# Optimization experiments

Measured on AMD Instinct MI355X. Metric: run time of the kernel, lower is better.

## Reference

```python
import jax, jax.numpy as jnp
import numpy as np

B, TT, TA, H = 2, 128, 512, 1024
EPS = 1e-5


def _conv1d(x, w, b, pad):
    # x: [B, C_in, T], w: [C_out, C_in, K] -> [B, C_out, T]
    y = jax.lax.conv_general_dilated(x, w, window_strides=(1,), padding=[(pad, pad)],
                                     dimension_numbers=('NCH', 'OIH', 'NCH'))
    return y + b[None, :, None]


def _groupnorm1(x, g, b):
    # GroupNorm(num_groups=1): normalize over (C, T) per sample. x: [B, C, T]
    mu = jnp.mean(x, axis=(1, 2), keepdims=True)
    var = jnp.var(x, axis=(1, 2), keepdims=True)
    xn = (x - mu) * jax.lax.rsqrt(var + EPS)
    return xn * g[None, :, None] + b[None, :, None]


def setup_inputs() -> dict:
    key = jax.random.key(0)
    ks = jax.random.split(key, 16)
    s = 0.02
    return {
        'text_hidden': jax.random.normal(ks[0], (B, TT, H), jnp.float32),
        'audio_hidden': jax.random.normal(ks[1], (B, TA, H), jnp.float32),
        # alignment_proj: Linear(2H, H) -> ReLU -> Linear(H, 1)
        'a_w1': jax.random.normal(ks[2], (2 * H, H), jnp.float32) * s,
        'a_b1': jnp.zeros((H,), jnp.float32),
        'a_w2': jax.random.normal(ks[3], (H, 1), jnp.float32) * s,
        'a_b2': jnp.zeros((1,), jnp.float32),
        # duration_predictor: Conv1d(H,H,3) ReLU GN(1,H) Conv1d(H,H,3) ReLU GN(1,H) Conv1d(H,1,1)
        'd_w1': jax.random.normal(ks[4], (H, H, 3), jnp.float32) * s,
        'd_b1': jnp.zeros((H,), jnp.float32),
        'gn1_g': jnp.ones((H,), jnp.float32),
        'gn1_b': jnp.zeros((H,), jnp.float32),
        'd_w2': jax.random.normal(ks[5], (H, H, 3), jnp.float32) * s,
        'd_b2': jnp.zeros((H,), jnp.float32),
        'gn2_g': jnp.ones((H,), jnp.float32),
        'gn2_b': jnp.zeros((H,), jnp.float32),
        'd_w3': jax.random.normal(ks[6], (1, H, 1), jnp.float32) * s,
        'd_b3': jnp.zeros((1,), jnp.float32),
    }


def reference(text_hidden, audio_hidden, a_w1, a_b1, a_w2, a_b2,
              d_w1, d_b1, gn1_g, gn1_b, d_w2, d_b2, gn2_g, gn2_b, d_w3, d_b3):
    # ---- predict_durations ----
    x = jnp.swapaxes(text_hidden, 1, 2)                      # [B, H, TT]
    x = _groupnorm1(jax.nn.relu(_conv1d(x, d_w1, d_b1, 1)), gn1_g, gn1_b)
    x = _groupnorm1(jax.nn.relu(_conv1d(x, d_w2, d_b2, 1)), gn2_g, gn2_b)
    x = _conv1d(x, d_w3, d_b3, 0)                            # [B, 1, TT]
    durations = jax.nn.softplus(x[:, 0, :])                  # [B, TT]

    # ---- soft_mas (temperature = 1.0) ----
    # Linear on concat([text, audio]) == text @ W1[:H] + audio @ W1[H:] + b1
    t_part = jnp.einsum('bth,hd->btd', text_hidden, a_w1[:H])    # [B, TT, H]
    a_part = jnp.einsum('bah,hd->bad', audio_hidden, a_w1[H:])   # [B, TA, H]
    hid = jax.nn.relu(t_part[:, :, None, :] + a_part[:, None, :, :] + a_b1)  # [B,TT,TA,H]
    logits = jnp.einsum('btad,do->bta', hid, a_w2) + a_b2[0]     # [B, TT, TA]

    pos = jnp.arange(TA, dtype=logits.dtype)                     # audio positions j
    expected = jnp.arange(TT, dtype=logits.dtype) * (TA / TT)    # expected pos per text i
    monotonic_bias = -0.1 * jnp.abs(pos[None, :] - expected[:, None])  # [TT, TA]
    logits = logits + monotonic_bias[None, :, :]

    alignment = jax.nn.softmax(logits, axis=-1)
    return alignment, durations
```

## Files before the change

### kernel.cpp

```cpp
#include <hip/hip_runtime.h>
#include <hip/hip_bf16.h>


typedef __bf16 bf16_t;
typedef __bf16 bf16x8 __attribute__((ext_vector_type(8)));
typedef __bf16 bf16x4 __attribute__((ext_vector_type(4)));
typedef float  f32x4  __attribute__((ext_vector_type(4)));
typedef _Float16 f16_t;
typedef _Float16 f16x2 __attribute__((ext_vector_type(2)));
typedef _Float16 f16x4 __attribute__((ext_vector_type(4)));

#define EPSV 1e-5f

#define OFF_TEXTBF   0u
#define OFF_AUDIOBF  524288u
#define OFF_W1TOP    2621440u
#define OFF_W1BOT    4718592u
#define OFF_WC1      6815744u
#define OFF_WC2      13107200u
#define OFF_TP       19398656u
#define OFF_W2F      19922944u
#define OFF_APT      20447232u
#define OFF_XP0      22544384u
#define OFF_XP1      23076864u
#define OFF_Y2       23609344u
#define OFF_BST1     24133632u
#define OFF_BST2     24137728u
#define OFF_LP       24141824u
#define OFF_SG       26238976u
#define OFF_SB       26251264u

__global__ __launch_bounds__(256) void prep_k(
    const float* __restrict__ text, const float* __restrict__ audio,
    const float* __restrict__ w1,
    const float* __restrict__ w1c, const float* __restrict__ w2c,
    const float* __restrict__ w2,
    const float* __restrict__ g1, const float* __restrict__ b1g,
    bf16_t* __restrict__ text_bf, bf16_t* __restrict__ xp0,
    bf16_t* __restrict__ audio_bf,
    bf16_t* __restrict__ topT, bf16_t* __restrict__ botT,
    bf16_t* __restrict__ wc1, bf16_t* __restrict__ wc2,
    bf16_t* __restrict__ xp1, f16_t* __restrict__ w2f,
    float* __restrict__ Sg, float* __restrict__ Sb)
{
    __shared__ float tile[32][33];
    const int bid = blockIdx.x;
    if (bid < 1280) {
        const int e = (bid * 256 + threadIdx.x) * 4;
        if (e < 262144) {
            float4 v = *(const float4*)&text[e];
            bf16x4 o; o[0] = (bf16_t)v.x; o[1] = (bf16_t)v.y; o[2] = (bf16_t)v.z; o[3] = (bf16_t)v.w;
            *(bf16x4*)&text_bf[e] = o;
            const int bt = e >> 10, h = e & 1023;
            const int b = bt >> 7, t = bt & 127;
            *(bf16x4*)&xp0[(size_t)(b * 130 + 1 + t) * 1024 + h] = o;
        } else {
            const int ea = e - 262144;
            float4 v = *(const float4*)&audio[ea];
            bf16x4 o; o[0] = (bf16_t)v.x; o[1] = (bf16_t)v.y; o[2] = (bf16_t)v.z; o[3] = (bf16_t)v.w;
            *(bf16x4*)&audio_bf[ea] = o;
        }
    } else if (bid < 3328) {
        const int b2 = bid - 1280;
        const int bx = b2 & 31, by = b2 >> 5;
        const int tx = threadIdx.x & 31, ty = threadIdx.x >> 5;
        #pragma unroll
        for (int j = 0; j < 4; ++j)
            tile[ty + j * 8][tx] = w1[(size_t)(by * 32 + ty + j * 8) * 1024 + bx * 32 + tx];
        __syncthreads();
        bf16_t* out = (by < 32) ? topT : botT;
        const int hbase = (by & 31) * 32;
        #pragma unroll
        for (int j = 0; j < 4; ++j) {
            const int d = bx * 32 + ty + j * 8;
            out[(size_t)d * 1024 + hbase + tx] = (bf16_t)tile[tx][ty + j * 8];
        }
    } else if (bid < 5376) {
        int b2 = bid - 3328;
        const int is2 = (b2 >= 1024) ? 1 : 0;
        const float* w = is2 ? w2c : w1c;
        bf16_t* wc = is2 ? wc2 : wc1;
        b2 &= 1023;
        const int o = b2, i4 = threadIdx.x;
        const float* src = w + (size_t)o * 3072 + i4 * 12;
        float4 v0 = *(const float4*)&src[0];
        float4 v1 = *(const float4*)&src[4];
        float4 v2 = *(const float4*)&src[8];
        const float f[12] = {v0.x, v0.y, v0.z, v0.w, v1.x, v1.y, v1.z, v1.w, v2.x, v2.y, v2.z, v2.w};
        float g4[4] = {1.f, 1.f, 1.f, 1.f}, bb4[4] = {0.f, 0.f, 0.f, 0.f};
        if (is2) {
            float4 gv = *(const float4*)&g1[i4 * 4];
            float4 bv = *(const float4*)&b1g[i4 * 4];
            g4[0] = gv.x; g4[1] = gv.y; g4[2] = gv.z; g4[3] = gv.w;
            bb4[0] = bv.x; bb4[1] = bv.y; bb4[2] = bv.z; bb4[3] = bv.w;
        }
        float sgr[3] = {0.f, 0.f, 0.f}, sbr[3] = {0.f, 0.f, 0.f};
        #pragma unroll
        for (int r = 0; r < 3; ++r) {
            bf16x4 o4;
            #pragma unroll
            for (int j = 0; j < 4; ++j) {
                const float wv = f[j * 3 + r];
                const float ws = wv * g4[j];
                sgr[r] += ws;
                sbr[r] += wv * bb4[j];
                o4[j] = (bf16_t)(is2 ? ws : wv);
            }
            *(bf16x4*)&wc[(size_t)r * 1048576 + (size_t)o * 1024 + i4 * 4] = o4;
        }
        if (is2) {
            #pragma unroll
            for (int off = 32; off > 0; off >>= 1) {
                #pragma unroll
                for (int r = 0; r < 3; ++r) {
                    sgr[r] += __shfl_xor(sgr[r], off);
                    sbr[r] += __shfl_xor(sbr[r], off);
                }
            }
            float* red = &tile[0][0];
            const int wid = threadIdx.x >> 6, lane = threadIdx.x & 63;
            if (lane == 0) {
                #pragma unroll
                for (int r = 0; r < 3; ++r) {
                    red[wid * 6 + r] = sgr[r];
                    red[wid * 6 + 3 + r] = sbr[r];
                }
            }
            __syncthreads();
            if (threadIdx.x < 6) {
                const float v = red[threadIdx.x] + red[6 + threadIdx.x]
                              + red[12 + threadIdx.x] + red[18 + threadIdx.x];
                if (threadIdx.x < 3) Sg[o * 3 + threadIdx.x] = v;
                else                 Sb[o * 3 + threadIdx.x - 3] = v;
            }
        }
    } else {
        const int tid = threadIdx.x;
        const int rowmap[4] = {0, 129, 130, 259};
        const int f = tid * 16;
        const int r = f >> 10, w = f & 1023;
        bf16x8 z8 = (bf16x8)(bf16_t)0.0f;
        bf16_t* p0 = xp0 + (size_t)rowmap[r] * 1024 + w;
        bf16_t* p1 = xp1 + (size_t)rowmap[r] * 1024 + w;
        *(bf16x8*)p0 = z8; *(bf16x8*)(p0 + 8) = z8;
        *(bf16x8*)p1 = z8; *(bf16x8*)(p1 + 8) = z8;
        float4 wv = *(const float4*)&w2[tid * 4];
        f16x4 wo; wo[0] = (f16_t)wv.x; wo[1] = (f16_t)wv.y; wo[2] = (f16_t)wv.z; wo[3] = (f16_t)wv.w;
        *(f16x4*)&w2f[tid * 4] = wo;
    }
}

__device__ __forceinline__ void conv_tile(
    const bf16_t* __restrict__ Wc, const bf16_t* __restrict__ xp,
    const float* __restrict__ bias, bf16_t* __restrict__ out,
    int rowsPerB, int rowOff, float* __restrict__ bstat, int statIdx,
    int bx, int by, int tid, float* smem, float* sred, float* sredq)
{
    const int w = tid >> 6, l = tid & 63;
    const int bt0 = bx * 32, m0 = by * 16;
    const int i0 = w * 128;
    const int lm = l & 15, lk = (l >> 4) * 8;
    const int b = bt0 >> 7, tbase = bt0 & 127;
    f32x4 acc0 = (f32x4)(0.0f), acc1 = (f32x4)(0.0f);
    const bf16_t* aq = Wc + (size_t)(m0 + lm) * 1024 + i0 + lk;
    const bf16_t* bq = xp + (size_t)(b * 130 + tbase + lm) * 1024 + i0 + lk;
    #pragma unroll
    for (int r = 0; r < 3; ++r) {
        const bf16_t* ar = aq + (size_t)r * 1048576;
        const bf16_t* br = bq + (size_t)r * 1024;
        #pragma unroll
        for (int kk = 0; kk < 128; kk += 32) {
            bf16x8 af = *(const bf16x8*)(ar + kk);
            bf16x8 bf0 = *(const bf16x8*)(br + kk);
            bf16x8 bf1 = *(const bf16x8*)(br + 16384 + kk);
            acc0 = __builtin_amdgcn_mfma_f32_16x16x32_bf16(af, bf0, acc0, 0, 0, 0);
            acc1 = __builtin_amdgcn_mfma_f32_16x16x32_bf16(af, bf1, acc1, 0, 0, 0);
        }
    }
    {
        const int row = (l >> 4) * 4;
        #pragma unroll
        for (int r = 0; r < 4; ++r) {
            smem[w * 576 + (row + r) * 36 + lm] = acc0[r];
            smem[w * 576 + (row + r) * 36 + 16 + lm] = acc1[r];
        }
    }
    __syncthreads();
    const int m = tid >> 5, n = tid & 31;
    float v = 0.f;
    #pragma unroll
    for (int ww = 0; ww < 8; ++ww) v += smem[ww * 576 + m * 36 + n];
    v = fmaxf(v + bias[m0 + m], 0.f);
    float s = v, q = v * v;
    __syncthreads();
    smem[m * 36 + n] = v;
    #pragma unroll
    for (int off = 32; off > 0; off >>= 1) {
        s += __shfl_xor(s, off);
        q += __shfl_xor(q, off);
    }
    if (l == 0) { sred[w] = s; sredq[w] = q; }
    __syncthreads();
    if (tid == 0) {
        float ts = 0.f, tq = 0.f;
        #pragma unroll
        for (int ww = 0; ww < 8; ++ww) { ts += sred[ww]; tq += sredq[ww]; }
        bstat[statIdx * 2] = ts;
        bstat[statIdx * 2 + 1] = tq;
    }
    if (tid < 64) {
        const int row = tid >> 1, half = tid & 1;
        bf16x8 o8;
        #pragma unroll
        for (int j = 0; j < 8; ++j) o8[j] = (bf16_t)smem[(half * 8 + j) * 36 + row];
        const int t = tbase + row;
        *(bf16x8*)&out[(size_t)(b * rowsPerB + rowOff + t) * 1024 + m0 + half * 8] = o8;
    }
}

__device__ __forceinline__ void reduce_bstat(
    const float* __restrict__ bstat, int b, int tid,
    float* sr, float* sq, float& mu, float& rsig)
{
    const int lane = tid & 63, wid = tid >> 6;
    float s = 0.f, q = 0.f;
    if (tid < 256) {
        float2 v = ((const float2*)bstat)[b * 256 + tid];
        s = v.x; q = v.y;
    }
    #pragma unroll
    for (int off = 32; off > 0; off >>= 1) {
        s += __shfl_xor(s, off);
        q += __shfl_xor(q, off);
    }
    if (lane == 0) { sr[wid] = s; sq[wid] = q; }
    __syncthreads();
    float ts = 0.f, tq = 0.f;
    #pragma unroll
    for (int i = 0; i < 8; ++i) { ts += sr[i]; tq += sq[i]; }
    const float cnt = 131072.f;
    mu = ts / cnt;
    const float var = tq / cnt - mu * mu;
    rsig = rsqrtf(var + EPSV);
}

__device__ __forceinline__ void conv2_tile(
    const bf16_t* __restrict__ Wc, const bf16_t* __restrict__ xp,
    const float* __restrict__ bias, bf16_t* __restrict__ out,
    const float* __restrict__ bstat1,
    const float* __restrict__ Sg, const float* __restrict__ Sb,
    float* __restrict__ bstat2, int statIdx,
    int bx, int by, int tid, float* smem, float* sred, float* sredq,
    float* sr, float* sq)
{
    const int w = tid >> 6, l = tid & 63;
    const int bt0 = bx * 32, m0 = by * 16;
    const int i0 = w * 128;
    const int lm = l & 15, lk = (l >> 4) * 8;
    const int b = bt0 >> 7, tbase = bt0 & 127;
    float mu1, rsig1;
    reduce_bstat(bstat1, b, tid, sr, sq, mu1, rsig1);
    f32x4 acc0 = (f32x4)(0.0f), acc1 = (f32x4)(0.0f);
    const bf16_t* aq = Wc + (size_t)(m0 + lm) * 1024 + i0 + lk;
    const bf16_t* bq = xp + (size_t)(b * 130 + tbase + lm) * 1024 + i0 + lk;
    #pragma unroll
    for (int r = 0; r < 3; ++r) {
        const bf16_t* ar = aq + (size_t)r * 1048576;
        const bf16_t* br = bq + (size_t)r * 1024;
        #pragma unroll
        for (int kk = 0; kk < 128; kk += 32) {
            bf16x8 af = *(const bf16x8*)(ar + kk);
            bf16x8 bf0 = *(const bf16x8*)(br + kk);
            bf16x8 bf1 = *(const bf16x8*)(br + 16384 + kk);
            acc0 = __builtin_amdgcn_mfma_f32_16x16x32_bf16(af, bf0, acc0, 0, 0, 0);
            acc1 = __builtin_amdgcn_mfma_f32_16x16x32_bf16(af, bf1, acc1, 0, 0, 0);
        }
    }
    {
        const int row = (l >> 4) * 4;
        #pragma unroll
        for (int r = 0; r < 4; ++r) {
            smem[w * 576 + (row + r) * 36 + lm] = acc0[r];
            smem[w * 576 + (row + r) * 36 + 16 + lm] = acc1[r];
        }
    }
    __syncthreads();
    const int m = tid >> 5, n = tid & 31;
    float v = 0.f;
    #pragma unroll
    for (int ww = 0; ww < 8; ++ww) v += smem[ww * 576 + m * 36 + n];
    const int o = m0 + m;
    const int tloc = tbase + n;
    float sb = Sb[o * 3] + Sb[o * 3 + 1] + Sb[o * 3 + 2];
    float sg = Sg[o * 3] + Sg[o * 3 + 1] + Sg[o * 3 + 2];
    if (tloc == 0)   { sb -= Sb[o * 3];     sg -= Sg[o * 3]; }
    if (tloc == 127) { sb -= Sb[o * 3 + 2]; sg -= Sg[o * 3 + 2]; }
    v = fmaxf(rsig1 * v + sb - mu1 * rsig1 * sg + bias[o], 0.f);
    float s = v, q = v * v;
    __syncthreads();
    smem[m * 36 + n] = v;
    #pragma unroll
    for (int off = 32; off > 0; off >>= 1) {
        s += __shfl_xor(s, off);
        q += __shfl_xor(q, off);
    }
    if (l == 0) { sred[w] = s; sredq[w] = q; }
    __syncthreads();
    if (tid == 0) {
        float ts = 0.f, tq = 0.f;
        #pragma unroll
        for (int ww = 0; ww < 8; ++ww) { ts += sred[ww]; tq += sredq[ww]; }
        bstat2[statIdx * 2] = ts;
        bstat2[statIdx * 2 + 1] = tq;
    }
    if (tid < 64) {
        const int row = tid >> 1, half = tid & 1;
        bf16x8 o8;
        #pragma unroll
        for (int j = 0; j < 8; ++j) o8[j] = (bf16_t)smem[(half * 8 + j) * 36 + row];
        const int t = tbase + row;
        *(bf16x8*)&out[(size_t)(b * 128 + t) * 1024 + m0 + half * 8] = o8;
    }
}

__device__ __forceinline__ void gemm_unit(
    int unit, int ut, float* base,
    const bf16_t* __restrict__ text_bf, const bf16_t* __restrict__ w1topT,
    const float* __restrict__ b1, f16_t* __restrict__ tp,
    const bf16_t* __restrict__ audio_bf, const bf16_t* __restrict__ w1botT,
    f16_t* __restrict__ apT4)
{
    const int is_tp = (unit < 256) ? 1 : 0;
    const int b2 = is_tp ? unit : unit - 256;
    const int n0 = (b2 & 31) * 32, m0 = (b2 >> 5) * 32;
    const int w = ut >> 6, l = ut & 63;
    const int lm = l & 15, lk = (l >> 4) * 8;
    const int k0 = w * 256;
    const bf16_t* A  = is_tp ? text_bf : audio_bf;
    const bf16_t* Bt = is_tp ? w1topT : w1botT;
    f32x4 acc[2][2];
    #pragma unroll
    for (int mt = 0; mt < 2; ++mt)
        #pragma unroll
        for (int nt = 0; nt < 2; ++nt) acc[mt][nt] = (f32x4)(0.0f);
    const bf16_t* Ap = A + (size_t)(m0 + lm) * 1024 + k0 + lk;
    const bf16_t* Bp = Bt + (size_t)(n0 + lm) * 1024 + k0 + lk;
    #pragma unroll
    for (int kk = 0; kk < 256; kk += 32) {
        bf16x8 af[2], bfr[2];
        #pragma unroll
        for (int i = 0; i < 2; ++i) af[i] = *(const bf16x8*)(Ap + (size_t)i * 16384 + kk);
        #pragma unroll
        for (int i = 0; i < 2; ++i) bfr[i] = *(const bf16x8*)(Bp + (size_t)i * 16384 + kk);
        #pragma unroll
        for (int mt = 0; mt < 2; ++mt)
            #pragma unroll
            for (int nt = 0; nt < 2; ++nt)
                acc[mt][nt] = __builtin_amdgcn_mfma_f32_16x16x32_bf16(af[mt], bfr[nt], acc[mt][nt], 0, 0, 0);
    }
    #pragma unroll
    for (int mt = 0; mt < 2; ++mt) {
        const int row = mt * 16 + (l >> 4) * 4;
        #pragma unroll
        for (int nt = 0; nt < 2; ++nt)
            #pragma unroll
            for (int r = 0; r < 4; ++r)
                base[w * 1152 + (row + r) * 36 + nt * 16 + lm] = acc[mt][nt][r];
    }
    __syncthreads();
    if (is_tp) {
        const int m = ut >> 3, n4 = (ut & 7) * 4;
        f16x4 v;
        #pragma unroll
        for (int j = 0; j < 4; ++j)
            v[j] = (f16_t)(base[m * 36 + n4 + j] + base[1152 + m * 36 + n4 + j]
                         + base[2304 + m * 36 + n4 + j] + base[3456 + m * 36 + n4 + j]
                         + b1[n0 + n4 + j]);
        *(f16x4*)&tp[(size_t)(m0 + m) * 1024 + n0 + n4] = v;
    } else {
        const int a = ut >> 3, q = ut & 7;
        const int b = m0 >> 9, a0 = m0 & 511;
        f16x4 v;
        #pragma unroll
        for (int c = 0; c < 4; ++c)
            v[c] = (f16_t)(base[a * 36 + q * 4 + c] + base[1152 + a * 36 + q * 4 + c]
                         + base[2304 + a * 36 + q * 4 + c] + base[3456 + a * 36 + q * 4 + c]);
        const size_t hq = (size_t)(n0 >> 2) + q;
        *(f16x4*)&apT4[(hq * 1024 + b * 512 + a0 + a) * 4] = v;
    }
}

__global__ __launch_bounds__(512, 4) void p2_k(
    const bf16_t* __restrict__ wc1, const bf16_t* __restrict__ xp0,
    const float* __restrict__ d_b1, bf16_t* __restrict__ xp1,
    float* __restrict__ bstat1,
    const bf16_t* __restrict__ text_bf, const bf16_t* __restrict__ w1topT,
    const float* __restrict__ a_b1, f16_t* __restrict__ tp,
    const bf16_t* __restrict__ audio_bf, const bf16_t* __restrict__ w1botT,
    f16_t* __restrict__ apT4)
{
    __shared__ float smem[9216];
    __shared__ float sred[8], sredq[8];
    const int bid = blockIdx.x;
    const int tid = threadIdx.x;
    if (bid < 512) {
        conv_tile(wc1, xp0, d_b1, xp1, 130, 1, bstat1, bid,
                  bid >> 6, bid & 63, tid, smem, sred, sredq);
    } else {
        const int unit = (bid - 512) * 2 + (tid >> 8);
        gemm_unit(unit, tid & 255, smem + (tid >> 8) * 4608,
                  text_bf, w1topT, a_b1, tp, audio_bf, w1botT, apT4);
    }
}

__device__ __forceinline__ float dot2_acc(f16x2 x, f16x2 w, float acc) {
#if __has_builtin(__builtin_amdgcn_fdot2)
    return __builtin_amdgcn_fdot2(x, w, acc, false);
#else
    return acc + (float)x[0] * (float)w[0] + (float)x[1] * (float)w[1];
#endif
}

__global__ __launch_bounds__(512, 4) void p3_k(
    const bf16_t* __restrict__ wc2, const bf16_t* __restrict__ xp1,
    const float* __restrict__ d_b2, bf16_t* __restrict__ y2,
    float* __restrict__ bstat2, const float* __restrict__ bstat1,
    const float* __restrict__ Sg, const float* __restrict__ Sb,
    const f16_t* __restrict__ tp, const f16_t* __restrict__ apT4,
    const f16_t* __restrict__ w2f, float* __restrict__ lp)
{
    __shared__ float smem[4608];
    __shared__ float sred[8], sredq[8], sr[8], sq[8];
    const int bid = blockIdx.x;
    const int tid = threadIdx.x;
    if (bid < 512) {
        conv2_tile(wc2, xp1, d_b2, y2, bstat1, Sg, Sb, bstat2, bid,
                   bid >> 6, bid & 63, tid, smem, sred, sredq, sr, sq);
    } else {
        const int lb = bid - 512;
        const int btp = lb & 63, hc = lb >> 6;
        const int bt0 = btp * 4;
        const int b = bt0 >> 7;
        const int a = tid;
        const f16_t* tpr = tp + (size_t)bt0 * 1024 + hc * 256;
        const f16_t* w2r = w2f + hc * 256;
        const f16_t* apc = apT4 + ((size_t)(hc * 64) * 1024 + b * 512 + a) * 4;
        float acc[4] = {0.f, 0.f, 0.f, 0.f};
        const f16x2 zero = (f16x2)(f16_t)0.0f;
        #pragma unroll 2
        for (int hq = 0; hq < 64; hq += 2) {
            f16x4 a0 = *(const f16x4*)(apc + (size_t)hq * 4096);
            f16x4 a1 = *(const f16x4*)(apc + (size_t)(hq + 1) * 4096);
            f16x4 w0 = *(const f16x4*)&w2r[hq * 4];
            f16x4 w1 = *(const f16x4*)&w2r[hq * 4 + 4];
            #pragma unroll
            for (int r = 0; r < 4; ++r) {
                f16x4 t0 = *(const f16x4*)&tpr[r * 1024 + hq * 4];
                f16x4 t1 = *(const f16x4*)&tpr[r * 1024 + hq * 4 + 4];
                f16x2 p;
                p = __builtin_elementwise_max((f16x2){t0[0] + a0[0], t0[1] + a0[1]}, zero);
                acc[r] = dot2_acc(p, (f16x2){w0[0], w0[1]}, acc[r]);
                p = __builtin_elementwise_max((f16x2){t0[2] + a0[2], t0[3] + a0[3]}, zero);
                acc[r] = dot2_acc(p, (f16x2){w0[2], w0[3]}, acc[r]);
                p = __builtin_elementwise_max((f16x2){t1[0] + a1[0], t1[1] + a1[1]}, zero);
                acc[r] = dot2_acc(p, (f16x2){w1[0], w1[1]}, acc[r]);
                p = __builtin_elementwise_max((f16x2){t1[2] + a1[2], t1[3] + a1[3]}, zero);
                acc[r] = dot2_acc(p, (f16x2){w1[2], w1[3]}, acc[r]);
            }
        }
        float* dst = lp + (size_t)(hc * 256 + bt0) * 512 + a;
        #pragma unroll
        for (int r = 0; r < 4; ++r) dst[(size_t)r * 512] = acc[r];
    }
}

__global__ __launch_bounds__(512) void combine_k(
    const float* __restrict__ lp, const float* __restrict__ b2,
    const bf16_t* __restrict__ y2, const float* __restrict__ bstat2,
    const float* __restrict__ g, const float* __restrict__ bet,
    const float* __restrict__ w3, const float* __restrict__ b3,
    float* __restrict__ out)
{
    __shared__ float redm[8], redsum[8];
    const int bid = blockIdx.x;
    const int tid = threadIdx.x;
    if (bid < 256) {
        const int bt = bid, t = bt & 127;
        const int a = tid;
        const int lane = a & 63, wid = a >> 6;
        const size_t base = (size_t)bt * 512 + a;
        float v = lp[base] + lp[131072 + base] + lp[262144 + base] + lp[393216 + base];
        v += b2[0] - 0.1f * fabsf((float)a - 4.0f * (float)t);
        float m = v;
        #pragma unroll
        for (int off = 32; off > 0; off >>= 1) m = fmaxf(m, __shfl_xor(m, off));
        if (lane == 0) redm[wid] = m;
        __syncthreads();
        float M = redm[0];
        #pragma unroll
        for (int i = 1; i < 8; ++i) M = fmaxf(M, redm[i]);
        const float e = expf(v - M);
        float s = e;
        #pragma unroll
        for (int off = 32; off > 0; off >>= 1) s += __shfl_xor(s, off);
        if (lane == 0) redsum[wid] = s;
        __syncthreads();
        float S = redsum[0];
        #pragma unroll
        for (int i = 1; i < 8; ++i) S += redsum[i];
        out[(size_t)bt * 512 + a] = e * (1.0f / S);
    } else {
        const int cb = bid - 256;
        const int b = (cb * 8) >> 7;
        float mu, rsig;
        reduce_bstat(bstat2, b, tid, redm, redsum, mu, rsig);
        const int lane = tid & 63, w = tid >> 6;
        const int bt = cb * 8 + w;
        const bf16_t* row = y2 + (size_t)bt * 1024 + lane * 16;
        float s1 = 0.f, s2 = 0.f, s3 = 0.f;
        #pragma unroll
        for (int c = 0; c < 2; ++c) {
            bf16x8 yv = *(const bf16x8*)(row + c * 8);
            #pragma unroll
            for (int j = 0; j < 8; ++j) {
                const int i = lane * 16 + c * 8 + j;
                const float gw = g[i] * w3[i];
                s1 += gw * (float)yv[j];
                s2 += gw;
                s3 += bet[i] * w3[i];
            }
        }
        #pragma unroll
        for (int off = 32; off > 0; off >>= 1) {
            s1 += __shfl_xor(s1, off);
            s2 += __shfl_xor(s2, off);
            s3 += __shfl_xor(s3, off);
        }
        if (lane == 0) {
            const float t = rsig * (s1 - mu * s2) + s3 + b3[0];
            out[131072 + bt] = fmaxf(t, 0.f) + log1pf(expf(-fabsf(t)));
        }
    }
}

extern "C" void kernel_launch(void* const* d_in, const int* in_sizes, int n_in,
                              void* d_out, int out_size, void* d_ws, size_t ws_size,
                              hipStream_t stream) {
    const float* text   = (const float*)d_in[0];
    const float* audio  = (const float*)d_in[1];
    const float* a_w1   = (const float*)d_in[2];
    const float* a_b1   = (const float*)d_in[3];
    const float* a_w2   = (const float*)d_in[4];
    const float* a_b2   = (const float*)d_in[5];
    const float* d_w1   = (const float*)d_in[6];
    const float* d_b1   = (const float*)d_in[7];
    const float* gn1_g  = (const float*)d_in[8];
    const float* gn1_b  = (const float*)d_in[9];
    const float* d_w2   = (const float*)d_in[10];
    const float* d_b2   = (const float*)d_in[11];
    const float* gn2_g  = (const float*)d_in[12];
    const float* gn2_b  = (const float*)d_in[13];
    const float* d_w3   = (const float*)d_in[14];
    const float* d_b3   = (const float*)d_in[15];

    char* ws = (char*)d_ws;
    float* outf = (float*)d_out;

    bf16_t* text_bf  = (bf16_t*)(ws + OFF_TEXTBF);
    bf16_t* audio_bf = (bf16_t*)(ws + OFF_AUDIOBF);
    bf16_t* w1topT   = (bf16_t*)(ws + OFF_W1TOP);
    bf16_t* w1botT   = (bf16_t*)(ws + OFF_W1BOT);
    bf16_t* wc1      = (bf16_t*)(ws + OFF_WC1);
    bf16_t* wc2      = (bf16_t*)(ws + OFF_WC2);
    f16_t*  tp       = (f16_t*) (ws + OFF_TP);
    f16_t*  w2f      = (f16_t*) (ws + OFF_W2F);
    f16_t*  apT4     = (f16_t*) (ws + OFF_APT);
    bf16_t* xp0      = (bf16_t*)(ws + OFF_XP0);
    bf16_t* xp1      = (bf16_t*)(ws + OFF_XP1);
    bf16_t* y2       = (bf16_t*)(ws + OFF_Y2);
    float*  bstat1   = (float*) (ws + OFF_BST1);
    float*  bstat2   = (float*) (ws + OFF_BST2);
    float*  lp       = (float*) (ws + OFF_LP);
    float*  Sgp      = (float*) (ws + OFF_SG);
    float*  Sbp      = (float*) (ws + OFF_SB);

    prep_k<<<dim3(5377), 256, 0, stream>>>(text, audio, a_w1, d_w1, d_w2, a_w2,
                                           gn1_g, gn1_b,
                                           text_bf, xp0, audio_bf, w1topT, w1botT,
                                           wc1, wc2, xp1, w2f, Sgp, Sbp);
    p2_k<<<dim3(1152), 512, 0, stream>>>(wc1, xp0, d_b1, xp1, bstat1,
                                         text_bf, w1topT, a_b1, tp,
                                         audio_bf, w1botT, apT4);
    p3_k<<<dim3(768), 512, 0, stream>>>(wc2, xp1, d_b2, y2, bstat2, bstat1,
                                        Sgp, Sbp, tp, apT4, w2f, lp);
    combine_k<<<dim3(288), 512, 0, stream>>>(lp, a_b2, y2, bstat2,
                                             gn2_g, gn2_b, d_w3, d_b3, outf);
}
```

Baseline: 181.6 us.

## Replace split-K block GEMMs with one full-K tile per wave, no LDS reduction

Measured after the change: 207.4 us. 1.14x slower.

```diff
diff --git a/kernel.cpp b/kernel.cpp
--- a/kernel.cpp
+++ b/kernel.cpp
@@ -29,6 +29,8 @@
 #define OFF_LP       24141824u
 #define OFF_SG       26238976u
 #define OFF_SB       26251264u
+#define OFF_SGF      26263552u
+#define OFF_SBF      26267648u
 
 __global__ __launch_bounds__(256) void prep_k(
     const float* __restrict__ text, const float* __restrict__ audio,
@@ -41,7 +43,8 @@
     bf16_t* __restrict__ topT, bf16_t* __restrict__ botT,
     bf16_t* __restrict__ wc1, bf16_t* __restrict__ wc2,
     bf16_t* __restrict__ xp1, f16_t* __restrict__ w2f,
-    float* __restrict__ Sg, float* __restrict__ Sb)
+    float* __restrict__ Sg, float* __restrict__ Sb,
+    float* __restrict__ SgF, float* __restrict__ SbF)
 {
     __shared__ float tile[32][33];
     const int bid = blockIdx.x;
@@ -132,7 +135,11 @@
                               + red[12 + threadIdx.x] + red[18 + threadIdx.x];
                 if (threadIdx.x < 3) Sg[o * 3 + threadIdx.x] = v;
                 else                 Sb[o * 3 + threadIdx.x - 3] = v;
-            }
+                red[24 + threadIdx.x] = v;
+            }
+            __syncthreads();
+            if (threadIdx.x == 0)      SgF[o] = red[24] + red[25] + red[26];
+            else if (threadIdx.x == 1) SbF[o] = red[27] + red[28] + red[29];
         }
     } else {
         const int tid = threadIdx.x;
@@ -150,26 +157,25 @@
     }
 }
 
-__device__ __forceinline__ void conv_tile(
+__device__ __forceinline__ float wave_red_add(float v) {
+    #pragma unroll
+    for (int off = 32; off > 0; off >>= 1) v += __shfl_xor(v, off);
+    return v;
+}
+
+__device__ __forceinline__ void conv_mfma(
     const bf16_t* __restrict__ Wc, const bf16_t* __restrict__ xp,
-    const float* __restrict__ bias, bf16_t* __restrict__ out,
-    int rowsPerB, int rowOff, float* __restrict__ bstat, int statIdx,
-    int bx, int by, int tid, float* smem, float* sred, float* sredq)
+    int m0, int b, int tbase, int l, f32x4& acc0, f32x4& acc1)
 {
-    const int w = tid >> 6, l = tid & 63;
-    const int bt0 = bx * 32, m0 = by * 16;
-    const int i0 = w * 128;
     const int lm = l & 15, lk = (l >> 4) * 8;
-    const int b = bt0 >> 7, tbase = bt0 & 127;
-    f32x4 acc0 = (f32x4)(0.0f), acc1 = (f32x4)(0.0f);
-    const bf16_t* aq = Wc + (size_t)(m0 + lm) * 1024 + i0 + lk;
-    const bf16_t* bq = xp + (size_t)(b * 130 + tbase + lm) * 1024 + i0 + lk;
+    const bf16_t* aq = Wc + (size_t)(m0 + lm) * 1024 + lk;
+    const bf16_t* bq = xp + (size_t)(b * 130 + tbase + lm) * 1024 + lk;
     #pragma unroll
     for (int r = 0; r < 3; ++r) {
         const bf16_t* ar = aq + (size_t)r * 1048576;
         const bf16_t* br = bq + (size_t)r * 1024;
-        #pragma unroll
-        for (int kk = 0; kk < 128; kk += 32) {
+        #pragma unroll 4
+        for (int kk = 0; kk < 1024; kk += 32) {
             bf16x8 af = *(const bf16x8*)(ar + kk);
             bf16x8 bf0 = *(const bf16x8*)(br + kk);
             bf16x8 bf1 = *(const bf16x8*)(br + 16384 + kk);
@@ -177,220 +183,9 @@
             acc1 = __builtin_amdgcn_mfma_f32_16x16x32_bf16(af, bf1, acc1, 0, 0, 0);
         }
     }
-    {
-        const int row = (l >> 4) * 4;
-        #pragma unroll
-        for (int r = 0; r < 4; ++r) {
-            smem[w * 576 + (row + r) * 36 + lm] = acc0[r];
-            smem[w * 576 + (row + r) * 36 + 16 + lm] = acc1[r];
-        }
-    }
-    __syncthreads();
-    const int m = tid >> 5, n = tid & 31;
-    float v = 0.f;
-    #pragma unroll
-    for (int ww = 0; ww < 8; ++ww) v += smem[ww * 576 + m * 36 + n];
-    v = fmaxf(v + bias[m0 + m], 0.f);
-    float s = v, q = v * v;
-    __syncthreads();
-    smem[m * 36 + n] = v;
-    #pragma unroll
-    for (int off = 32; off > 0; off >>= 1) {
-        s += __shfl_xor(s, off);
-        q += __shfl_xor(q, off);
-    }
-    if (l == 0) { sred[w] = s; sredq[w] = q; }
-    __syncthreads();
-    if (tid == 0) {
-        float ts = 0.f, tq = 0.f;
-        #pragma unroll
-        for (int ww = 0; ww < 8; ++ww) { ts += sred[ww]; tq += sredq[ww]; }
-        bstat[statIdx * 2] = ts;
-        bstat[statIdx * 2 + 1] = tq;
-    }
-    if (tid < 64) {
-        const int row = tid >> 1, half = tid & 1;
-        bf16x8 o8;
-        #pragma unroll
-        for (int j = 0; j < 8; ++j) o8[j] = (bf16_t)smem[(half * 8 + j) * 36 + row];
-        const int t = tbase + row;
-        *(bf16x8*)&out[(size_t)(b * rowsPerB + rowOff + t) * 1024 + m0 + half * 8] = o8;
-    }
-}
-
-__device__ __forceinline__ void reduce_bstat(
-    const float* __restrict__ bstat, int b, int tid,
-    float* sr, float* sq, float& mu, float& rsig)
-{
-    const int lane = tid & 63, wid = tid >> 6;
-    float s = 0.f, q = 0.f;
-    if (tid < 256) {
-        float2 v = ((const float2*)bstat)[b * 256 + tid];
-        s = v.x; q = v.y;
-    }
-    #pragma unroll
-    for (int off = 32; off > 0; off >>= 1) {
-        s += __shfl_xor(s, off);
-        q += __shfl_xor(q, off);
-    }
-    if (lane == 0) { sr[wid] = s; sq[wid] = q; }
-    __syncthreads();
-    float ts = 0.f, tq = 0.f;
-    #pragma unroll
-    for (int i = 0; i < 8; ++i) { ts += sr[i]; tq += sq[i]; }
-    const float cnt = 131072.f;
-    mu = ts / cnt;
-    const float var = tq / cnt - mu * mu;
-    rsig = rsqrtf(var + EPSV);
-}
-
-__device__ __forceinline__ void conv2_tile(
-    const bf16_t* __restrict__ Wc, const bf16_t* __restrict__ xp,
-    const float* __restrict__ bias, bf16_t* __restrict__ out,
-    const float* __restrict__ bstat1,
-    const float* __restrict__ Sg, const float* __restrict__ Sb,
-    float* __restrict__ bstat2, int statIdx,
-    int bx, int by, int tid, float* smem, float* sred, float* sredq,
-    float* sr, float* sq)
-{
-    const int w = tid >> 6, l = tid & 63;
-    const int bt0 = bx * 32, m0 = by * 16;
-    const int i0 = w * 128;
-    const int lm = l & 15, lk = (l >> 4) * 8;
-    const int b = bt0 >> 7, tbase = bt0 & 127;
-    float mu1, rsig1;
-    reduce_bstat(bstat1, b, tid, sr, sq, mu1, rsig1);
-    f32x4 acc0 = (f32x4)(0.0f), acc1 = (f32x4)(0.0f);
-    const bf16_t* aq = Wc + (size_t)(m0 + lm) * 1024 + i0 + lk;
-    const bf16_t* bq = xp + (size_t)(b * 130 + tbase + lm) * 1024 + i0 + lk;
-    #pragma unroll
-    for (int r = 0; r < 3; ++r) {
-        const bf16_t* ar = aq + (size_t)r * 1048576;
-        const bf16_t* br = bq + (size_t)r * 1024;
-        #pragma unroll
-        for (int kk = 0; kk < 128; kk += 32) {
-            bf16x8 af = *(const bf16x8*)(ar + kk);
-            bf16x8 bf0 = *(const bf16x8*)(br + kk);
-            bf16x8 bf1 = *(const bf16x8*)(br + 16384 + kk);
-            acc0 = __builtin_amdgcn_mfma_f32_16x16x32_bf16(af, bf0, acc0, 0, 0, 0);
-            acc1 = __builtin_amdgcn_mfma_f32_16x16x32_bf16(af, bf1, acc1, 0, 0, 0);
-        }
-    }
-    {
-        const int row = (l >> 4) * 4;
-        #pragma unroll
-        for (int r = 0; r < 4; ++r) {
-            smem[w * 576 + (row + r) * 36 + lm] = acc0[r];
-            smem[w * 576 + (row + r) * 36 + 16 + lm] = acc1[r];
-        }
-    }
-    __syncthreads();
-    const int m = tid >> 5, n = tid & 31;
-    float v = 0.f;
-    #pragma unroll
-    for (int ww = 0; ww < 8; ++ww) v += smem[ww * 576 + m * 36 + n];
-    const int o = m0 + m;
-    const int tloc = tbase + n;
-    float sb = Sb[o * 3] + Sb[o * 3 + 1] + Sb[o * 3 + 2];
-    float sg = Sg[o * 3] + Sg[o * 3 + 1] + Sg[o * 3 + 2];
-    if (tloc == 0)   { sb -= Sb[o * 3];     sg -= Sg[o * 3]; }
-    if (tloc == 127) { sb -= Sb[o * 3 + 2]; sg -= Sg[o * 3 + 2]; }
-    v = fmaxf(rsig1 * v + sb - mu1 * rsig1 * sg + bias[o], 0.f);
-    float s = v, q = v * v;
-    __syncthreads();
-    smem[m * 36 + n] = v;
-    #pragma unroll
-    for (int off = 32; off > 0; off >>= 1) {
-        s += __shfl_xor(s, off);
-        q += __shfl_xor(q, off);
-    }
-    if (l == 0) { sred[w] = s; sredq[w] = q; }
-    __syncthreads();
-    if (tid == 0) {
-        float ts = 0.f, tq = 0.f;
-        #pragma unroll
-        for (int ww = 0; ww < 8; ++ww) { ts += sred[ww]; tq += sredq[ww]; }
-        bstat2[statIdx * 2] = ts;
-        bstat2[statIdx * 2 + 1] = tq;
-    }
-    if (tid < 64) {
-        const int row = tid >> 1, half = tid & 1;
-        bf16x8 o8;
-        #pragma unroll
-        for (int j = 0; j < 8; ++j) o8[j] = (bf16_t)smem[(half * 8 + j) * 36 + row];
-        const int t = tbase + row;
-        *(bf16x8*)&out[(size_t)(b * 128 + t) * 1024 + m0 + half * 8] = o8;
-    }
-}
-
-__device__ __forceinline__ void gemm_unit(
-    int unit, int ut, float* base,
-    const bf16_t* __restrict__ text_bf, const bf16_t* __restrict__ w1topT,
-    const float* __restrict__ b1, f16_t* __restrict__ tp,
-    const bf16_t* __restrict__ audio_bf, const bf16_t* __restrict__ w1botT,
-    f16_t* __restrict__ apT4)
-{
-    const int is_tp = (unit < 256) ? 1 : 0;
-    const int b2 = is_tp ? unit : unit - 256;
-    const int n0 = (b2 & 31) * 32, m0 = (b2 >> 5) * 32;
-    const int w = ut >> 6, l = ut & 63;
-    const int lm = l & 15, lk = (l >> 4) * 8;
-    const int k0 = w * 256;
-    const bf16_t* A  = is_tp ? text_bf : audio_bf;
-    const bf16_t* Bt = is_tp ? w1topT : w1botT;
-    f32x4 acc[2][2];
-    #pragma unroll
-    for (int mt = 0; mt < 2; ++mt)
-        #pragma unroll
-        for (int nt = 0; nt < 2; ++nt) acc[mt][nt] = (f32x4)(0.0f);
-    const bf16_t* Ap = A + (size_t)(m0 + lm) * 1024 + k0 + lk;
-    const bf16_t* Bp = Bt + (size_t)(n0 + lm) * 1024 + k0 + lk;
-    #pragma unroll
-    for (int kk = 0; kk < 256; kk += 32) {
-        bf16x8 af[2], bfr[2];
-        #pragma unroll
-        for (int i = 0; i < 2; ++i) af[i] = *(const bf16x8*)(Ap + (size_t)i * 16384 + kk);
-        #pragma unroll
-        for (int i = 0; i < 2; ++i) bfr[i] = *(const bf16x8*)(Bp + (size_t)i * 16384 + kk);
-        #pragma unroll
-        for (int mt = 0; mt < 2; ++mt)
-            #pragma unroll
-            for (int nt = 0; nt < 2; ++nt)
-                acc[mt][nt] = __builtin_amdgcn_mfma_f32_16x16x32_bf16(af[mt], bfr[nt], acc[mt][nt], 0, 0, 0);
-    }
-    #pragma unroll
-    for (int mt = 0; mt < 2; ++mt) {
-        const int row = mt * 16 + (l >> 4) * 4;
-        #pragma unroll
-        for (int nt = 0; nt < 2; ++nt)
-            #pragma unroll
-            for (int r = 0; r < 4; ++r)
-                base[w * 1152 + (row + r) * 36 + nt * 16 + lm] = acc[mt][nt][r];
-    }
-    __syncthreads();
-    if (is_tp) {
-        const int m = ut >> 3, n4 = (ut & 7) * 4;
-        f16x4 v;
-        #pragma unroll
-        for (int j = 0; j < 4; ++j)
-            v[j] = (f16_t)(base[m * 36 + n4 + j] + base[1152 + m * 36 + n4 + j]
-                         + base[2304 + m * 36 + n4 + j] + base[3456 + m * 36 + n4 + j]
-                         + b1[n0 + n4 + j]);
-        *(f16x4*)&tp[(size_t)(m0 + m) * 1024 + n0 + n4] = v;
-    } else {
-        const int a = ut >> 3, q = ut & 7;
-        const int b = m0 >> 9, a0 = m0 & 511;
-        f16x4 v;
-        #pragma unroll
-        for (int c = 0; c < 4; ++c)
-            v[c] = (f16_t)(base[a * 36 + q * 4 + c] + base[1152 + a * 36 + q * 4 + c]
-                         + base[2304 + a * 36 + q * 4 + c] + base[3456 + a * 36 + q * 4 + c]);
-        const size_t hq = (size_t)(n0 >> 2) + q;
-        *(f16x4*)&apT4[(hq * 1024 + b * 512 + a0 + a) * 4] = v;
-    }
-}
-
-__global__ __launch_bounds__(512, 4) void p2_k(
+}
+
+__global__ __launch_bounds__(256) void p2_k(
     const bf16_t* __restrict__ wc1, const bf16_t* __restrict__ xp0,
     const float* __restrict__ d_b1, bf16_t* __restrict__ xp1,
     float* __restrict__ bstat1,
@@ -399,17 +194,93 @@
     const bf16_t* __restrict__ audio_bf, const bf16_t* __restrict__ w1botT,
     f16_t* __restrict__ apT4)
 {
-    __shared__ float smem[9216];
-    __shared__ float sred[8], sredq[8];
     const int bid = blockIdx.x;
-    const int tid = threadIdx.x;
-    if (bid < 512) {
-        conv_tile(wc1, xp0, d_b1, xp1, 130, 1, bstat1, bid,
-                  bid >> 6, bid & 63, tid, smem, sred, sredq);
+    const int wv = threadIdx.x >> 6, l = threadIdx.x & 63;
+    const int lm = l & 15, lh = l >> 4, lk = lh * 8;
+    if (bid < 128) {
+        const int tile = bid * 4 + wv;
+        const int bx = tile >> 6, by = tile & 63;
+        const int bt0 = bx * 32, m0 = by * 16;
+        const int b = bt0 >> 7, tbase = bt0 & 127;
+        f32x4 acc0 = (f32x4)(0.0f), acc1 = (f32x4)(0.0f);
+        conv_mfma(wc1, xp0, m0, b, tbase, l, acc0, acc1);
+        float4 bv = *(const float4*)&d_b1[m0 + lh * 4];
+        float s = 0.f, q = 0.f;
+        #pragma unroll
+        for (int t2 = 0; t2 < 2; ++t2) {
+            f32x4 a = t2 ? acc1 : acc0;
+            bf16x4 o4;
+            #pragma unroll
+            for (int r = 0; r < 4; ++r) {
+                float v = fmaxf(a[r] + ((const float*)&bv)[r], 0.f);
+                s += v; q += v * v;
+                o4[r] = (bf16_t)v;
+            }
+            const int bt = tbase + t2 * 16 + lm;
+            *(bf16x4*)&xp1[(size_t)(b * 130 + 1 + bt) * 1024 + m0 + lh * 4] = o4;
+        }
+        s = wave_red_add(s); q = wave_red_add(q);
+        if (l == 0) { bstat1[tile * 2] = s; bstat1[tile * 2 + 1] = q; }
     } else {
-        const int unit = (bid - 512) * 2 + (tid >> 8);
-        gemm_unit(unit, tid & 255, smem + (tid >> 8) * 4608,
-                  text_bf, w1topT, a_b1, tp, audio_bf, w1botT, apT4);
+        const bf16_t *At, *Bm;
+        int h0, r0, is_tp;
+        if (bid < 192) {
+            const int unit = (bid - 128) * 4 + wv;
+            h0 = (unit & 31) * 32; r0 = (unit >> 5) * 32;
+            At = w1topT; Bm = text_bf; is_tp = 1;
+        } else {
+            const int unit = (bid - 192) * 4 + wv;
+            h0 = (unit & 31) * 32; r0 = (unit >> 5) * 32;
+            At = w1botT; Bm = audio_bf; is_tp = 0;
+        }
+        f32x4 acc[2][2];
+        #pragma unroll
+        for (int mt = 0; mt < 2; ++mt)
+            #pragma unroll
+            for (int nt = 0; nt < 2; ++nt) acc[mt][nt] = (f32x4)(0.0f);
+        const bf16_t* Ap = At + (size_t)(h0 + lm) * 1024 + lk;
+        const bf16_t* Bp = Bm + (size_t)(r0 + lm) * 1024 + lk;
+        #pragma unroll 4
+        for (int kk = 0; kk < 1024; kk += 32) {
+            bf16x8 af0 = *(const bf16x8*)(Ap + kk);
+            bf16x8 af1 = *(const bf16x8*)(Ap + 16384 + kk);
+            bf16x8 bf0 = *(const bf16x8*)(Bp + kk);
+            bf16x8 bf1 = *(const bf16x8*)(Bp + 16384 + kk);
+            acc[0][0] = __builtin_amdgcn_mfma_f32_16x16x32_bf16(af0, bf0, acc[0][0], 0, 0, 0);
+            acc[0][1] = __builtin_amdgcn_mfma_f32_16x16x32_bf16(af0, bf1, acc[0][1], 0, 0, 0);
+            acc[1][0] = __builtin_amdgcn_mfma_f32_16x16x32_bf16(af1, bf0, acc[1][0], 0, 0, 0);
+            acc[1][1] = __builtin_amdgcn_mfma_f32_16x16x32_bf16(af1, bf1, acc[1][1], 0, 0, 0);
+        }
+        if (is_tp) {
+            #pragma unroll
+            for (int mt = 0; mt < 2; ++mt) {
+                const int hb = h0 + mt * 16 + lh * 4;
+                float4 bv = *(const float4*)&a_b1[hb];
+                #pragma unroll
+                for (int nt = 0; nt < 2; ++nt) {
+                    const int bt = r0 + nt * 16 + lm;
+                    f16x4 v;
+                    #pragma unroll
+                    for (int r = 0; r < 4; ++r)
+                        v[r] = (f16_t)(acc[mt][nt][r] + ((const float*)&bv)[r]);
+                    *(f16x4*)&tp[(size_t)bt * 1024 + hb] = v;
+                }
+            }
+        } else {
+            #pragma unroll
+            for (int mt = 0; mt < 2; ++mt) {
+                const int hq = (h0 + mt * 16 + lh * 4) >> 2;
+                #pragma unroll
+                for (int nt = 0; nt < 2; ++nt) {
+                    const int aa = r0 + nt * 16 + lm;
+                    const int bb = aa >> 9, al = aa & 511;
+                    f16x4 v;
+                    #pragma unroll
+                    for (int r = 0; r < 4; ++r) v[r] = (f16_t)acc[mt][nt][r];
+                    *(f16x4*)&apT4[((size_t)hq * 1024 + bb * 512 + al) * 4] = v;
+                }
+            }
+        }
     }
 }
 
@@ -421,27 +292,66 @@
 #endif
 }
 
-__global__ __launch_bounds__(512, 4) void p3_k(
+__global__ __launch_bounds__(256) void p3_k(
     const bf16_t* __restrict__ wc2, const bf16_t* __restrict__ xp1,
     const float* __restrict__ d_b2, bf16_t* __restrict__ y2,
     float* __restrict__ bstat2, const float* __restrict__ bstat1,
-    const float* __restrict__ Sg, const float* __restrict__ Sb,
+    const float* __restrict__ SgF, const float* __restrict__ SbF,
+    const float* __restrict__ Sg3, const float* __restrict__ Sb3,
     const f16_t* __restrict__ tp, const f16_t* __restrict__ apT4,
     const f16_t* __restrict__ w2f, float* __restrict__ lp)
 {
-    __shared__ float smem[4608];
-    __shared__ float sred[8], sredq[8], sr[8], sq[8];
     const int bid = blockIdx.x;
     const int tid = threadIdx.x;
-    if (bid < 512) {
-        conv2_tile(wc2, xp1, d_b2, y2, bstat1, Sg, Sb, bstat2, bid,
-                   bid >> 6, bid & 63, tid, smem, sred, sredq, sr, sq);
+    if (bid < 128) {
+        const int wv = tid >> 6, l = tid & 63;
+        const int lm = l & 15, lh = l >> 4;
+        const int tile = bid * 4 + wv;
+        const int bx = tile >> 6, by = tile & 63;
+        const int bt0 = bx * 32, m0 = by * 16;
+        const int b = bt0 >> 7, tbase = bt0 & 127;
+        f32x4 acc0 = (f32x4)(0.0f), acc1 = (f32x4)(0.0f);
+        conv_mfma(wc2, xp1, m0, b, tbase, l, acc0, acc1);
+        float s0, q0;
+        {
+            const float4* bp = (const float4*)bstat1 + (size_t)b * 128;
+            float4 p0 = bp[l * 2], p1 = bp[l * 2 + 1];
+            s0 = p0.x + p0.z + p1.x + p1.z;
+            q0 = p0.y + p0.w + p1.y + p1.w;
+        }
+        s0 = wave_red_add(s0); q0 = wave_red_add(q0);
+        const float mu = s0 * (1.f / 131072.f);
+        const float rsig = rsqrtf(q0 * (1.f / 131072.f) - mu * mu + EPSV);
+        float4 bv = *(const float4*)&d_b2[m0 + lh * 4];
+        float4 gF = *(const float4*)&SgF[m0 + lh * 4];
+        float4 bF = *(const float4*)&SbF[m0 + lh * 4];
+        float s = 0.f, q = 0.f;
+        #pragma unroll
+        for (int t2 = 0; t2 < 2; ++t2) {
+            f32x4 a = t2 ? acc1 : acc0;
+            const int bt = tbase + t2 * 16 + lm;
+            const bool e0 = (bt == 0), e1 = (bt == 127);
+            bf16x4 o4;
+            #pragma unroll
+            for (int r = 0; r < 4; ++r) {
+                const int o = m0 + lh * 4 + r;
+                float sg = ((const float*)&gF)[r], sb = ((const float*)&bF)[r];
+                if (e0) { sg -= Sg3[o * 3];     sb -= Sb3[o * 3]; }
+                if (e1) { sg -= Sg3[o * 3 + 2]; sb -= Sb3[o * 3 + 2]; }
+                float v = fmaxf(rsig * a[r] + sb - mu * rsig * sg + ((const float*)&bv)[r], 0.f);
+                s += v; q += v * v;
+                o4[r] = (bf16_t)v;
+            }
+            *(bf16x4*)&y2[(size_t)(b * 128 + bt) * 1024 + m0 + lh * 4] = o4;
+        }
+        s = wave_red_add(s); q = wave_red_add(q);
+        if (l == 0) { bstat2[tile * 2] = s; bstat2[tile * 2 + 1] = q; }
     } else {
-        const int lb = bid - 512;
-        const int btp = lb & 63, hc = lb >> 6;
+        const int lb = bid - 128;
+        const int hc = lb >> 7, btp = (lb >> 1) & 63, half = lb & 1;
         const int bt0 = btp * 4;
         const int b = bt0 >> 7;
-        const int a = tid;
+        const int a = half * 256 + tid;
         const f16_t* tpr = tp + (size_t)bt0 * 1024 + hc * 256;
         const f16_t* w2r = w2f + hc * 256;
         const f16_t* apc = apT4 + ((size_t)(hc * 64) * 1024 + b * 512 + a) * 4;
@@ -472,6 +382,32 @@
         #pragma unroll
         for (int r = 0; r < 4; ++r) dst[(size_t)r * 512] = acc[r];
     }
+}
+
+__device__ __forceinline__ void reduce_bstat(
+    const float* __restrict__ bstat, int b, int tid,
+    float* sr, float* sq, float& mu, float& rsig)
+{
+    const int lane = tid & 63, wid = tid >> 6;
+    float s = 0.f, q = 0.f;
+    if (tid < 256) {
+        float2 v = ((const float2*)bstat)[b * 256 + tid];
+        s = v.x; q = v.y;
+    }
+    #pragma unroll
+    for (int off = 32; off > 0; off >>= 1) {
+        s += __shfl_xor(s, off);
+        q += __shfl_xor(q, off);
+    }
+    if (lane == 0) { sr[wid] = s; sq[wid] = q; }
+    __syncthreads();
+    float ts = 0.f, tq = 0.f;
+    #pragma unroll
+    for (int i = 0; i < 8; ++i) { ts += sr[i]; tq += sq[i]; }
+    const float cnt = 131072.f;
+    mu = ts / cnt;
+    const float var = tq / cnt - mu * mu;
+    rsig = rsqrtf(var + EPSV);
 }
 
 __global__ __launch_bounds__(512) void combine_k(
@@ -581,18 +517,21 @@
     float*  bstat1   = (float*) (ws + OFF_BST1);
     float*  bstat2   = (float*) (ws + OFF_BST2);
     float*  lp       = (float*) (ws + OFF_LP);
-    float*  Sgp      = (float*) (ws + OFF_SG);
-    float*  Sbp      = (float*) (ws + OFF_SB);
+    float*  Sg3     = (float*) (ws + OFF_SG);
+    float*  Sb3     = (float*) (ws + OFF_SB);
+    float*  SgFp    = (float*) (ws + OFF_SGF);
+    float*  SbFp    = (float*) (ws + OFF_SBF);
 
     prep_k<<<dim3(5377), 256, 0, stream>>>(text, audio, a_w1, d_w1, d_w2, a_w2,
                                            gn1_g, gn1_b,
                                            text_bf, xp0, audio_bf, w1topT, w1botT,
-                                           wc1, wc2, xp1, w2f, Sgp, Sbp);
-    p2_k<<<dim3(1152), 512, 0, stream>>>(wc1, xp0, d_b1, xp1, bstat1,
-                                         text_bf, w1topT, a_b1, tp,
-                                         audio_bf, w1botT, apT4);
-    p3_k<<<dim3(768), 512, 0, stream>>>(wc2, xp1, d_b2, y2, bstat2, bstat1,
-                                        Sgp, Sbp, tp, apT4, w2f, lp);
+                                           wc1, wc2, xp1, w2f, Sg3, Sb3,
+                                           SgFp, SbFp);
+    p2_k<<<dim3(448), 256, 0, stream>>>(wc1, xp0, d_b1, xp1, bstat1,
+                                        text_bf, w1topT, a_b1, tp,
+                                        audio_bf, w1botT, apT4);
+    p3_k<<<dim3(640), 256, 0, stream>>>(wc2, xp1, d_b2, y2, bstat2, bstat1,
+                                        SgFp, SbFp, Sg3, Sb3, tp, apT4, w2f, lp);
     combine_k<<<dim3(288), 512, 0, stream>>>(lp, a_b2, y2, bstat2,
                                              gn2_g, gn2_b, d_w3, d_b3, outf);
 }
```
